# Performance work log

Measured on AMD Instinct MI355X. Metric: run time of the kernel, lower is better.

The kernel has to match this reference:

```python
import jax, jax.numpy as jnp
import numpy as np

M, B, S, D, H = 3, 32, 256, 768, 1024
LN_EPS = 1e-5


def _ln(x, g, b):
    m = jnp.mean(x, axis=-1, keepdims=True)
    v = jnp.mean((x - m) ** 2, axis=-1, keepdims=True)
    return (x - m) / jnp.sqrt(v + LN_EPS) * g + b


def setup_inputs() -> dict:
    key = jax.random.key(0)
    ks = jax.random.split(key, 16)
    sc = 0.02  # weight init scale
    return {
        "feats": jax.random.normal(ks[0], (M, B, S, D), jnp.float32),
        "Wq": jax.random.normal(ks[1], (M, D, D), jnp.float32) * sc,
        "bq": jnp.zeros((M, D), jnp.float32),
        "Wk": jax.random.normal(ks[2], (M, D, D), jnp.float32) * sc,
        "bk": jnp.zeros((M, D), jnp.float32),
        "Wv": jax.random.normal(ks[3], (M, D, D), jnp.float32) * sc,
        "bv": jnp.zeros((M, D), jnp.float32),
        "pgq_w": jax.random.normal(ks[4], (M, D), jnp.float32) * sc,
        "pgq_b": jnp.zeros((M,), jnp.float32),
        "pgk_w": jax.random.normal(ks[5], (M, D), jnp.float32) * sc,
        "pgk_b": jnp.zeros((M,), jnp.float32),
        "mu_w": jax.random.normal(ks[6], (M, D), jnp.float32) * sc,
        "mu_b": jnp.zeros((M,), jnp.float32),
        "lv_w": jax.random.normal(ks[7], (M, D), jnp.float32) * sc,
        "lv_b": jnp.zeros((M,), jnp.float32),
        "dyn": jnp.ones((1,), jnp.float32),
        "WE_w": jax.random.normal(ks[8], (M, D, D), jnp.float32) * sc,
        "WE_b": jnp.zeros((M, D), jnp.float32),
        "Wh_w": jax.random.normal(ks[9], (M, D, D), jnp.float32) * sc,
        "Wh_b": jnp.zeros((M, D), jnp.float32),
        "Wqc_w": jax.random.normal(ks[10], (M, D, D), jnp.float32) * sc,
        "Wqc_b": jnp.zeros((M, D), jnp.float32),
        "lnE_g": jnp.ones((M, D), jnp.float32),
        "lnE_b": jnp.zeros((M, D), jnp.float32),
        "lnG_g": jnp.ones((M, D), jnp.float32),
        "lnG_b": jnp.zeros((M, D), jnp.float32),
        "out_w": jax.random.normal(ks[11], (D * M, H), jnp.float32) * sc,
        "out_b": jnp.zeros((H,), jnp.float32),
        "eps": jax.random.normal(ks[12], (M, M - 1, B, S, 1), jnp.float32),
    }


def reference(feats, Wq, bq, Wk, bk, Wv, bv, pgq_w, pgq_b, pgk_w, pgk_b,
              mu_w, mu_b, lv_w, lv_b, dyn, WE_w, WE_b, Wh_w, Wh_b, Wqc_w, Wqc_b,
              lnE_g, lnE_b, lnG_g, lnG_b, out_w, out_b, eps):
    # batched per-modality projections: [M,B,S,D]
    Qs = jnp.einsum('mbsd,mde->mbse', feats, Wq) + bq[:, None, None, :]
    Ks = jnp.einsum('mbsd,mde->mbse', feats, Wk) + bk[:, None, None, :]
    Vs = jnp.einsum('mbsd,mde->mbse', feats, Wv) + bv[:, None, None, :]
    scale = 1.0 / jnp.sqrt(jnp.float32(D))

    kl = jnp.float32(0.0)
    outs = []
    for i in range(M):
        Qi = Qs[i]  # [B,S,D]
        mu = jnp.einsum('bsd,d->bs', Qi, mu_w[i])[..., None] + mu_b[i]      # [B,S,1]
        lv = jnp.einsum('bsd,d->bs', Qi, lv_w[i])[..., None] + lv_b[i]      # [B,S,1]
        std = jnp.exp(0.5 * lv)
        pq_base = jax.nn.sigmoid(
            jnp.einsum('bsd,d->bs', Qi, pgq_w[i])[..., None] + pgq_b[i])    # [B,S,1]
        kl_i = -0.5 * jnp.sum(1.0 + lv - mu ** 2 - jnp.exp(lv))
        agg = jnp.zeros_like(Qi)
        cnt = 0
        for j in range(M):
            if j == i:
                continue
            d_gate = mu + dyn * std * eps[i, cnt]  # reparameterization
            cnt += 1
            kl = kl + kl_i
            g = jax.nn.sigmoid(d_gate)             # [B,S,1]
            p_q = pq_base * g
            p_k = jax.nn.sigmoid(
                jnp.einsum('bsd,d->bs', Ks[j], pgk_w[i])[..., None] + pgk_b[i]) * g
            A = jnp.einsum('bqd,bkd->bqk', Qi, Ks[j]) * scale
            A = A * p_q * jnp.swapaxes(p_k, 1, 2)  # pregated scores
            W = jax.nn.softmax(A, axis=-1)
            agg = agg + jnp.einsum('bqk,bkd->bqd', W, Vs[j])
        # CAG
        E = jax.nn.relu(agg @ WE_w[i] + WE_b[i])
        G = jax.nn.relu(agg @ Wh_w[i] + Wh_b[i] + Qi @ Wqc_w[i] + Wqc_b[i])
        Ci = _ln(E, lnE_g[i], lnE_b[i]) * _ln(G, lnG_g[i], lnG_b[i])
        outs.append(Ci)
    fused = jnp.concatenate(outs, axis=-1)[:, 0, :]  # [B, M*D]
    out = fused @ out_w + out_b                       # [B, H]
    return out, kl
```

## Files before the change

### kernel.cpp

```cpp
#include <hip/hip_runtime.h>

#define M 3
#define B 32
#define S 256
#define D 768
#define H 1024
#define MD (M * D)
#define NP (M * (M - 1))
#define SCALE 0.03608439182435161f
#define LN_EPS 1e-5f

#define OFF_WMU   0
#define OFF_WLV   2304
#define OFF_WPGQ  4608
#define OFF_WPK   6912
#define OFF_CMU   11520
#define OFF_CLV   11523
#define OFF_CPGQ  11526
#define OFF_CPK   11529
#define OFF_MU    11552
#define OFF_LV    36128
#define OFF_PKPRE 60704
#define OFF_PQPRE 109856
#define OFF_Q     109952
#define OFF_QBK   183680
#define OFF_QK    183872
#define OFF_FSUM  331328
#define OFF_AGG   478784
#define OFF_E     552512
#define OFF_G     626240
#define OFF_FUSED 699968
#define OFF_KL    773696
#define OFF_WKT   773760
#define OFF_ARENA 2543232

__device__ __forceinline__ float wave_reduce(float v) {
    #pragma unroll
    for (int o = 32; o > 0; o >>= 1) v += __shfl_down(v, o, 64);
    return v;
}

__device__ __forceinline__ float sigmoidf(float x) {
    return 1.0f / (1.0f + __expf(-x));
}

__device__ __forceinline__ float dot4(float4 a, float4 b) {
    return a.x * b.x + a.y * b.y + a.z * b.z + a.w * b.w;
}

__device__ __forceinline__ void fma4(float4& a, float s, float4 w) {
    a.x += s * w.x; a.y += s * w.y; a.z += s * w.z; a.w += s * w.w;
}

__global__ __launch_bounds__(256) void k_prep(const float* Wq, const float* Wk,
        const float* bq, const float* bk,
        const float* mu_w, const float* mu_b, const float* lv_w, const float* lv_b,
        const float* pgq_w, const float* pgq_b, const float* pgk_w, const float* pgk_b,
        float* ws) {
    int blk = blockIdx.x;
    if (blk < 72) {
        int mat = blk / 12, rg = blk % 12;
        const float* Wm; const float *va, *vb, *vc;
        float *oa, *ob, *oc; int nv;
        if (mat < 3) {
            int i = mat;
            Wm = Wq + i * D * D;
            va = mu_w + i * D; vb = lv_w + i * D; vc = pgq_w + i * D;
            oa = ws + OFF_WMU + i * D; ob = ws + OFF_WLV + i * D; oc = ws + OFF_WPGQ + i * D;
            nv = 3;
        } else {
            int j = mat - 3;
            int i1 = (j == 0) ? 1 : 0, i2 = (j == 2) ? 1 : 2;
            int p1 = 2 * i1 + ((j < i1) ? j : j - 1);
            int p2 = 2 * i2 + ((j < i2) ? j : j - 1);
            Wm = Wk + j * D * D;
            va = pgk_w + i1 * D; vb = pgk_w + i2 * D; vc = va;
            oa = ws + OFF_WPK + p1 * D; ob = ws + OFF_WPK + p2 * D; oc = oa;
            nv = 2;
        }
        int wave = threadIdx.x >> 6, lane = threadIdx.x & 63;
        const float4* va4 = (const float4*)va;
        const float4* vb4 = (const float4*)vb;
        const float4* vc4 = (const float4*)vc;
        float4 A0 = va4[lane], A1 = va4[lane + 64], A2 = va4[lane + 128];
        float4 B0 = vb4[lane], B1 = vb4[lane + 64], B2 = vb4[lane + 128];
        float4 C0 = vc4[lane], C1 = vc4[lane + 64], C2 = vc4[lane + 128];
        int base = rg * 64 + wave * 16;
        for (int r = 0; r < 16; r += 2) {
            const float4* rowP = (const float4*)(Wm + (base + r) * D);
            const float4* rowQ = (const float4*)(Wm + (base + r + 1) * D);
            float4 x0 = rowP[lane], x1 = rowP[lane + 64], x2 = rowP[lane + 128];
            float4 y0 = rowQ[lane], y1 = rowQ[lane + 64], y2 = rowQ[lane + 128];
            float daP = dot4(x0, A0) + dot4(x1, A1) + dot4(x2, A2);
            float dbP = dot4(x0, B0) + dot4(x1, B1) + dot4(x2, B2);
            float dcP = dot4(x0, C0) + dot4(x1, C1) + dot4(x2, C2);
            float daQ = dot4(y0, A0) + dot4(y1, A1) + dot4(y2, A2);
            float dbQ = dot4(y0, B0) + dot4(y1, B1) + dot4(y2, B2);
            float dcQ = dot4(y0, C0) + dot4(y1, C1) + dot4(y2, C2);
            daP = wave_reduce(daP); dbP = wave_reduce(dbP);
            daQ = wave_reduce(daQ); dbQ = wave_reduce(dbQ);
            if (nv == 3) { dcP = wave_reduce(dcP); dcQ = wave_reduce(dcQ); }
            if (lane == 0) {
                oa[base + r] = daP; ob[base + r] = dbP;
                oa[base + r + 1] = daQ; ob[base + r + 1] = dbQ;
                if (nv == 3) { oc[base + r] = dcP; oc[base + r + 1] = dcQ; }
            }
        }
    } else if (blk < 87) {
        int job = blk - 72;
        const float *a, *bvec; float bias; float* out;
        if (job < 3)      { int i = job;     a = bq + i * D; bvec = mu_w + i * D;  bias = mu_b[i];  out = ws + OFF_CMU + i; }
        else if (job < 6) { int i = job - 3; a = bq + i * D; bvec = lv_w + i * D;  bias = lv_b[i];  out = ws + OFF_CLV + i; }
        else if (job < 9) { int i = job - 6; a = bq + i * D; bvec = pgq_w + i * D; bias = pgq_b[i]; out = ws + OFF_CPGQ + i; }
        else {
            int p = job - 9, i = p / 2, c = p % 2, j = c + (c >= i ? 1 : 0);
            a = bk + j * D; bvec = pgk_w + i * D; bias = pgk_b[i]; out = ws + OFF_CPK + p;
        }
        int t = threadIdx.x;
        float part = 0.f;
        if (t < 192) part = dot4(((const float4*)a)[t], ((const float4*)bvec)[t]);
        part = wave_reduce(part);
        __shared__ float r[4];
        if ((t & 63) == 0) r[t >> 6] = part;
        __syncthreads();
        if (t == 0) *out = r[0] + r[1] + r[2] + r[3] + bias;
    } else {
        int r = blk - 87;
        int j = r / 144; r = r % 144;
        int d0 = (r / 12) * 64, e0 = (r % 12) * 64;
        __shared__ float tile[64][65];
        const float* src = Wk + j * D * D;
        for (int idx = threadIdx.x; idx < 4096; idx += 256) {
            int rr = idx / 64, cc = idx % 64;
            tile[rr][cc] = src[(d0 + rr) * D + e0 + cc];
        }
        __syncthreads();
        float* dst = ws + OFF_WKT + j * D * D;
        for (int idx = threadIdx.x; idx < 4096; idx += 256) {
            int rr = idx / 64, cc = idx % 64;
            dst[(e0 + rr) * D + d0 + cc] = tile[cc][rr];
        }
    }
}

__global__ __launch_bounds__(256) void k_stats(const float* feats, float* ws) {
    __shared__ float klred[4];
    int wave = threadIdx.x >> 6, lane = threadIdx.x & 63;
    int m = blockIdx.x / 512;
    int row0 = blockIdx.x * 16 + wave * 4;
    int i1 = (m == 0) ? 1 : 0, i2 = (m == 2) ? 1 : 2;
    int p0 = 2 * i1 + ((m < i1) ? m : m - 1);
    int p1 = 2 * i2 + ((m < i2) ? m : m - 1);
    const float4* wmu  = (const float4*)(ws + OFF_WMU + m * D);
    const float4* wlv  = (const float4*)(ws + OFF_WLV + m * D);
    const float4* wpgq = (const float4*)(ws + OFF_WPGQ + m * D);
    const float4* wpk0 = (const float4*)(ws + OFF_WPK + p0 * D);
    const float4* wpk1 = (const float4*)(ws + OFF_WPK + p1 * D);
    float4 U0 = wmu[lane],  U1 = wmu[lane + 64],  U2 = wmu[lane + 128];
    float4 L0 = wlv[lane],  L1 = wlv[lane + 64],  L2 = wlv[lane + 128];
    float4 Q0 = wpgq[lane], Q1 = wpgq[lane + 64], Q2 = wpgq[lane + 128];
    float4 P0 = wpk0[lane], P1 = wpk0[lane + 64], P2 = wpk0[lane + 128];
    float4 R0 = wpk1[lane], R1 = wpk1[lane + 64], R2 = wpk1[lane + 128];
    float4 x[4][3];
    #pragma unroll
    for (int rr = 0; rr < 4; rr++) {
        const float4* f = (const float4*)(feats + (size_t)(row0 + rr) * D);
        x[rr][0] = f[lane]; x[rr][1] = f[lane + 64]; x[rr][2] = f[lane + 128];
    }
    float amu[4], alv[4], apgq[4], apk0[4], apk1[4];
    #pragma unroll
    for (int rr = 0; rr < 4; rr++) {
        amu[rr]  = dot4(x[rr][0], U0) + dot4(x[rr][1], U1) + dot4(x[rr][2], U2);
        alv[rr]  = dot4(x[rr][0], L0) + dot4(x[rr][1], L1) + dot4(x[rr][2], L2);
        apgq[rr] = dot4(x[rr][0], Q0) + dot4(x[rr][1], Q1) + dot4(x[rr][2], Q2);
        apk0[rr] = dot4(x[rr][0], P0) + dot4(x[rr][1], P1) + dot4(x[rr][2], P2);
        apk1[rr] = dot4(x[rr][0], R0) + dot4(x[rr][1], R1) + dot4(x[rr][2], R2);
    }
    #pragma unroll
    for (int rr = 0; rr < 4; rr++) {
        amu[rr] = wave_reduce(amu[rr]);  alv[rr] = wave_reduce(alv[rr]);
        apgq[rr] = wave_reduce(apgq[rr]);
        apk0[rr] = wave_reduce(apk0[rr]); apk1[rr] = wave_reduce(apk1[rr]);
    }
    if (lane == 0) {
        float cmu = ws[OFF_CMU + m], clv = ws[OFF_CLV + m];
        float cpgq = ws[OFF_CPGQ + m];
        float cpk0 = ws[OFF_CPK + p0], cpk1 = ws[OFF_CPK + p1];
        float klsum = 0.f;
        #pragma unroll
        for (int rr = 0; rr < 4; rr++) {
            int row = row0 + rr;
            int rem = row % (B * S);
            int b = rem / S, s = rem % S;
            float muv = amu[rr] + cmu;
            float lvv = alv[rr] + clv;
            ws[OFF_MU + row] = muv;
            ws[OFF_LV + row] = lvv;
            ws[OFF_PKPRE + (p0 * B + b) * S + s] = apk0[rr] + cpk0;
            ws[OFF_PKPRE + (p1 * B + b) * S + s] = apk1[rr] + cpk1;
            if (s == 0) ws[OFF_PQPRE + m * B + b] = apgq[rr] + cpgq;
            klsum += 1.0f + lvv - muv * muv - __expf(lvv);
        }
        klred[wave] = klsum;
    }
    __syncthreads();
    if (threadIdx.x == 0)
        atomicAdd(ws + OFF_KL, -(klred[0] + klred[1] + klred[2] + klred[3]));
}


__global__ __launch_bounds__(192) void k_qrow(const float* feats, const float* Wq, float* ws) {
    int blk = blockIdx.x;
    int i = blk / 96, r = blk % 96, bg = r / 24, kc = r % 24;
    int kbase = kc * 32;
    __shared__ __align__(16) float xs[32][8];
    for (int idx = threadIdx.x; idx < 256; idx += 192) {
        int d = idx / 8, bb = idx % 8;
        xs[d][bb] = feats[((size_t)(i * B + bg * 8 + bb) * S) * D + kbase + d];
    }
    __syncthreads();
    int e4 = threadIdx.x * 4;
    const float* Wm = Wq + i * D * D + kbase * D + e4;
    float4 acc[8];
    #pragma unroll
    for (int bb = 0; bb < 8; bb++) acc[bb] = make_float4(0.f, 0.f, 0.f, 0.f);
    for (int k = 0; k < 32; k++) {
        float4 w = *(const float4*)(Wm + k * D);
        float4 x0 = *(const float4*)&xs[k][0];
        float4 x1 = *(const float4*)&xs[k][4];
        fma4(acc[0], x0.x, w); fma4(acc[1], x0.y, w);
        fma4(acc[2], x0.z, w); fma4(acc[3], x0.w, w);
        fma4(acc[4], x1.x, w); fma4(acc[5], x1.y, w);
        fma4(acc[6], x1.z, w); fma4(acc[7], x1.w, w);
    }
    #pragma unroll
    for (int bb = 0; bb < 8; bb++)
        *(float4*)&ws[OFF_ARENA + kc * 73728 + (i * 32 + bg * 8 + bb) * 768 + e4] = acc[bb];
}

__global__ __launch_bounds__(256) void k_red_q(const float* bq, const float* bk, float* ws) {
    int blk = blockIdx.x;
    int i = blk / B, b = blk % B;
    int fbase = (i * B + b) * D;
    int t = threadIdx.x;
    __shared__ float4 qsh[192];
    __shared__ float redsh[8];
    if (t < 192) {
        float4 a = *(const float4*)&bq[i * D + t * 4];
        #pragma unroll
        for (int kc = 0; kc < 24; kc++) {
            float4 v = *(const float4*)&ws[OFF_ARENA + kc * 73728 + fbase + t * 4];
            a.x += v.x; a.y += v.y; a.z += v.z; a.w += v.w;
        }
        *(float4*)&ws[OFF_Q + fbase + t * 4] = a;
        qsh[t] = a;
    }
    __syncthreads();
    int jA = (i == 0) ? 1 : 0, jB = (i == 2) ? 1 : 2;
    float pA_ = 0.f, pB_ = 0.f;
    if (t < 192) {
        float4 q = qsh[t];
        pA_ = dot4(q, *(const float4*)&bk[jA * D + t * 4]);
        pB_ = dot4(q, *(const float4*)&bk[jB * D + t * 4]);
    }
    pA_ = wave_reduce(pA_); pB_ = wave_reduce(pB_);
    int wave = t >> 6, lane = t & 63;
    if (lane == 0) { redsh[wave] = pA_; redsh[4 + wave] = pB_; }
    __syncthreads();
    if (t == 0) {
        ws[OFF_QBK + (2 * i) * B + b]     = redsh[0] + redsh[1] + redsh[2] + redsh[3];
        ws[OFF_QBK + (2 * i + 1) * B + b] = redsh[4] + redsh[5] + redsh[6] + redsh[7];
    }
}

__global__ __launch_bounds__(192) void k_qk(float* ws) {
    int blk = blockIdx.x;
    int j = blk / 96, r = blk % 96, vg = r / 12, kc = r % 12;
    int kbase = kc * 64;
    int i1 = (j == 0) ? 1 : 0, i2 = (j == 2) ? 1 : 2;
    __shared__ __align__(16) float xs[64][8];
    for (int idx = threadIdx.x; idx < 512; idx += 192) {
        int d = idx / 8, v = idx % 8;
        int v64 = vg * 8 + v;
        int i_ = (v64 < 32) ? i1 : i2, b = v64 & 31;
        xs[d][v] = ws[OFF_Q + (i_ * 32 + b) * 768 + kbase + d];
    }
    __syncthreads();
    int e4 = threadIdx.x * 4;
    const float* Wm = ws + OFF_WKT + j * D * D + kbase * D + e4;
    float4 acc[8];
    #pragma unroll
    for (int bb = 0; bb < 8; bb++) acc[bb] = make_float4(0.f, 0.f, 0.f, 0.f);
// ... 299 lines not shown
    const float* gg = lnG_g + i * D; const float* gbv = lnG_b + i * D;
    o[t]       = ((e0 - mE) * sE * eg[t]       + ebv[t])       * ((g0 - mG) * sG * gg[t]       + gbv[t]);
    o[t + 256] = ((e1 - mE) * sE * eg[t + 256] + ebv[t + 256]) * ((g1 - mG) * sG * gg[t + 256] + gbv[t + 256]);
    o[t + 512] = ((e2 - mE) * sE * eg[t + 512] + ebv[t + 512]) * ((g2 - mG) * sG * gg[t + 512] + gbv[t + 512]);
}

__global__ __launch_bounds__(256) void k_out(const float* out_w, float* ws) {
    int blk = blockIdx.x;
    int bg = blk / 36, kc = blk % 36;
    int kbase = kc * 64;
    __shared__ __align__(16) float xs[64][8];
    for (int idx = threadIdx.x; idx < 512; idx += 256) {
        int d = idx / 8, bb = idx % 8;
        xs[d][bb] = ws[OFF_FUSED + (bg * 8 + bb) * MD + kbase + d];
    }
    __syncthreads();
    int e4 = threadIdx.x * 4;
    const float* Wm = out_w + kbase * H + e4;
    float4 acc[8];
    #pragma unroll
    for (int bb = 0; bb < 8; bb++) acc[bb] = make_float4(0.f, 0.f, 0.f, 0.f);
    for (int k = 0; k < 64; k++) {
        float4 w = *(const float4*)(Wm + k * H);
        float4 x0 = *(const float4*)&xs[k][0];
        float4 x1 = *(const float4*)&xs[k][4];
        fma4(acc[0], x0.x, w); fma4(acc[1], x0.y, w);
        fma4(acc[2], x0.z, w); fma4(acc[3], x0.w, w);
        fma4(acc[4], x1.x, w); fma4(acc[5], x1.y, w);
        fma4(acc[6], x1.z, w); fma4(acc[7], x1.w, w);
    }
    #pragma unroll
    for (int bb = 0; bb < 8; bb++)
        *(float4*)&ws[OFF_ARENA + kc * 32768 + (bg * 8 + bb) * 1024 + e4] = acc[bb];
}

__global__ __launch_bounds__(256) void k_fin(const float* out_b, float* ws, float* out) {
    int b = blockIdx.x;
    int h4 = threadIdx.x * 4;
    float4 a = *(const float4*)&out_b[h4];
    #pragma unroll
    for (int kc = 0; kc < 36; kc++) {
        float4 p = *(const float4*)&ws[OFF_ARENA + kc * 32768 + b * 1024 + h4];
        a.x += p.x; a.y += p.y; a.z += p.z; a.w += p.w;
    }
    *(float4*)&out[b * H + h4] = a;
    if (b == 0 && threadIdx.x == 0) out[B * H] = ws[OFF_KL];
}

extern "C" void kernel_launch(void* const* d_in, const int* in_sizes, int n_in,
                              void* d_out, int out_size, void* d_ws, size_t ws_size,
                              hipStream_t stream) {
    const float* feats = (const float*)d_in[0];
    const float* Wq    = (const float*)d_in[1];
    const float* bq    = (const float*)d_in[2];
    const float* Wk    = (const float*)d_in[3];
    const float* bk    = (const float*)d_in[4];
    const float* Wv    = (const float*)d_in[5];
    const float* bv    = (const float*)d_in[6];
    const float* pgq_w = (const float*)d_in[7];
    const float* pgq_b = (const float*)d_in[8];
    const float* pgk_w = (const float*)d_in[9];
    const float* pgk_b = (const float*)d_in[10];
    const float* mu_w  = (const float*)d_in[11];
    const float* mu_b  = (const float*)d_in[12];
    const float* lv_w  = (const float*)d_in[13];
    const float* lv_b  = (const float*)d_in[14];
    const float* dyn   = (const float*)d_in[15];
    const float* WE_w  = (const float*)d_in[16];
    const float* WE_b  = (const float*)d_in[17];
    const float* Wh_w  = (const float*)d_in[18];
    const float* Wh_b  = (const float*)d_in[19];
    const float* Wqc_w = (const float*)d_in[20];
    const float* Wqc_b = (const float*)d_in[21];
    const float* lnE_g = (const float*)d_in[22];
    const float* lnE_b = (const float*)d_in[23];
    const float* lnG_g = (const float*)d_in[24];
    const float* lnG_b = (const float*)d_in[25];
    const float* out_w = (const float*)d_in[26];
    const float* out_b = (const float*)d_in[27];
    const float* eps   = (const float*)d_in[28];
    float* ws  = (float*)d_ws;
    float* out = (float*)d_out;

    hipMemsetAsync((char*)d_ws + OFF_KL * sizeof(float), 0, sizeof(float), stream);

    k_prep<<<519, 256, 0, stream>>>(Wq, Wk, bq, bk, mu_w, mu_b, lv_w, lv_b,
                                    pgq_w, pgq_b, pgk_w, pgk_b, ws);
    k_stats<<<1536, 256, 0, stream>>>(feats, ws);
    k_qrow<<<288, 192, 0, stream>>>(feats, Wq, ws);
    k_red_q<<<96, 256, 0, stream>>>(bq, bk, ws);
    k_qk<<<288, 192, 0, stream>>>(ws);
    k_red_qk<<<144, 256, 0, stream>>>(ws);
    k_score<<<384, 256, 0, stream>>>(feats, ws);
    k_wsum<<<288, 256, 0, stream>>>(feats, eps, dyn, ws);
    k_agg<<<288, 192, 0, stream>>>(Wv, ws);
    k_red_agg<<<72, 256, 0, stream>>>(bv, ws);
    k_eg<<<288, 192, 0, stream>>>(WE_w, Wh_w, Wqc_w, ws);
    k_red_eg<<<144, 256, 0, stream>>>(WE_b, Wh_b, Wqc_b, ws);
    k_ln<<<M * B, 256, 0, stream>>>(lnE_g, lnE_b, lnG_g, lnG_b, ws);
    k_out<<<144, 256, 0, stream>>>(out_w, ws);
    k_fin<<<32, 256, 0, stream>>>(out_b, ws, out);
}
```

Baseline: 360.9 us.

## Fuse all stages into one cooperative persistent kernel with grid syncs

Replaces the chain of fifteen separate kernel launches with a single cooperative kernel that walks every former stage in grid-stride loops, separated by grid.sync barriers. It also folds the per-row statistics pass (mu, logvar, key-gate pre-activations, KL) into the score pass, so the large feats tensor is streamed once there instead of twice. The aim is to remove per-launch overhead and one full read of feats. The cost is fixed-size grid parallelism (512 blocks), grid-wide barrier latency between stages, and a fallback to the old launch chain if the cooperative launch fails.

```diff
diff --git a/kernel.cpp b/kernel.cpp
--- a/kernel.cpp
+++ b/kernel.cpp
@@ -1,4 +1,7 @@
 #include <hip/hip_runtime.h>
+#include <hip/hip_cooperative_groups.h>
+
+namespace cg = cooperative_groups;
 
 #define M 3
 #define B 32
@@ -51,6 +54,596 @@
 __device__ __forceinline__ void fma4(float4& a, float s, float4 w) {
     a.x += s * w.x; a.y += s * w.y; a.z += s * w.z; a.w += s * w.w;
 }
+
+struct MegaParams {
+    const float *feats, *Wq, *bq, *Wk, *bk, *Wv, *bv;
+    const float *pgq_w, *pgq_b, *pgk_w, *pgk_b;
+    const float *mu_w, *mu_b, *lv_w, *lv_b, *dyn;
+    const float *WE_w, *WE_b, *Wh_w, *Wh_b, *Wqc_w, *Wqc_b;
+    const float *lnE_g, *lnE_b, *lnG_g, *lnG_b, *out_w, *out_b, *eps;
+    float *ws, *out;
+};
+
+__global__ __launch_bounds__(256, 2) void k_mega(MegaParams p) {
+    cg::grid_group grid = cg::this_grid();
+    __shared__ __align__(16) char shraw[64 * 65 * 4];
+    float* ws = p.ws;
+    const int tid = threadIdx.x;
+    const int NB = gridDim.x;
+
+    if (blockIdx.x == 0 && tid == 0) ws[OFF_KL] = 0.f;
+
+    for (int vb = blockIdx.x; vb < 519; vb += NB) {
+        if (vb < 72) {
+            int mat = vb / 12, rg = vb % 12;
+            const float* Wm; const float *va, *vbv, *vc;
+            float *oa, *ob, *oc; int nv;
+            if (mat < 3) {
+                int i = mat;
+                Wm = p.Wq + i * D * D;
+                va = p.mu_w + i * D; vbv = p.lv_w + i * D; vc = p.pgq_w + i * D;
+                oa = ws + OFF_WMU + i * D; ob = ws + OFF_WLV + i * D; oc = ws + OFF_WPGQ + i * D;
+                nv = 3;
+            } else {
+                int j = mat - 3;
+                int i1 = (j == 0) ? 1 : 0, i2 = (j == 2) ? 1 : 2;
+                int p1 = 2 * i1 + ((j < i1) ? j : j - 1);
+                int p2 = 2 * i2 + ((j < i2) ? j : j - 1);
+                Wm = p.Wk + j * D * D;
+                va = p.pgk_w + i1 * D; vbv = p.pgk_w + i2 * D; vc = va;
+                oa = ws + OFF_WPK + p1 * D; ob = ws + OFF_WPK + p2 * D; oc = oa;
+                nv = 2;
+            }
+            int wave = tid >> 6, lane = tid & 63;
+            const float4* va4 = (const float4*)va;
+            const float4* vb4 = (const float4*)vbv;
+            const float4* vc4 = (const float4*)vc;
+            float4 A0 = va4[lane], A1 = va4[lane + 64], A2 = va4[lane + 128];
+            float4 B0 = vb4[lane], B1 = vb4[lane + 64], B2 = vb4[lane + 128];
+            float4 C0 = vc4[lane], C1 = vc4[lane + 64], C2 = vc4[lane + 128];
+            int base = rg * 64 + wave * 16;
+            for (int r = 0; r < 16; r += 2) {
+                const float4* rowP = (const float4*)(Wm + (base + r) * D);
+                const float4* rowQ = (const float4*)(Wm + (base + r + 1) * D);
+                float4 x0 = rowP[lane], x1 = rowP[lane + 64], x2 = rowP[lane + 128];
+                float4 y0 = rowQ[lane], y1 = rowQ[lane + 64], y2 = rowQ[lane + 128];
+                float daP = dot4(x0, A0) + dot4(x1, A1) + dot4(x2, A2);
+                float dbP = dot4(x0, B0) + dot4(x1, B1) + dot4(x2, B2);
+                float dcP = dot4(x0, C0) + dot4(x1, C1) + dot4(x2, C2);
+                float daQ = dot4(y0, A0) + dot4(y1, A1) + dot4(y2, A2);
+                float dbQ = dot4(y0, B0) + dot4(y1, B1) + dot4(y2, B2);
+                float dcQ = dot4(y0, C0) + dot4(y1, C1) + dot4(y2, C2);
+                daP = wave_reduce(daP); dbP = wave_reduce(dbP);
+                daQ = wave_reduce(daQ); dbQ = wave_reduce(dbQ);
+                if (nv == 3) { dcP = wave_reduce(dcP); dcQ = wave_reduce(dcQ); }
+                if (lane == 0) {
+                    oa[base + r] = daP; ob[base + r] = dbP;
+                    oa[base + r + 1] = daQ; ob[base + r + 1] = dbQ;
+                    if (nv == 3) { oc[base + r] = dcP; oc[base + r + 1] = dcQ; }
+                }
+            }
+        } else if (vb < 87) {
+            int job = vb - 72;
+            const float *a, *bvec; float bias; float* out;
+            if (job < 3)      { int i = job;     a = p.bq + i * D; bvec = p.mu_w + i * D;  bias = p.mu_b[i];  out = ws + OFF_CMU + i; }
+            else if (job < 6) { int i = job - 3; a = p.bq + i * D; bvec = p.lv_w + i * D;  bias = p.lv_b[i];  out = ws + OFF_CLV + i; }
+            else if (job < 9) { int i = job - 6; a = p.bq + i * D; bvec = p.pgq_w + i * D; bias = p.pgq_b[i]; out = ws + OFF_CPGQ + i; }
+            else {
+                int pp = job - 9, i = pp / 2, c = pp % 2, j = c + (c >= i ? 1 : 0);
+                a = p.bk + j * D; bvec = p.pgk_w + i * D; bias = p.pgk_b[i]; out = ws + OFF_CPK + pp;
+            }
+            float part = 0.f;
+            if (tid < 192) part = dot4(((const float4*)a)[tid], ((const float4*)bvec)[tid]);
+            part = wave_reduce(part);
+            float* rsh = (float*)shraw;
+            if ((tid & 63) == 0) rsh[tid >> 6] = part;
+            __syncthreads();
+            if (tid == 0) *out = rsh[0] + rsh[1] + rsh[2] + rsh[3] + bias;
+        } else {
+            int r = vb - 87;
+            int j = r / 144; r = r % 144;
+            int d0 = (r / 12) * 64, e0 = (r % 12) * 64;
+            float* tile = (float*)shraw;
+            const float* src = p.Wk + j * D * D;
+            for (int idx = tid; idx < 4096; idx += 256) {
+                int rr = idx / 64, cc = idx % 64;
+                tile[rr * 65 + cc] = src[(d0 + rr) * D + e0 + cc];
+            }
+            __syncthreads();
+            float* dst = ws + OFF_WKT + j * D * D;
+            for (int idx = tid; idx < 4096; idx += 256) {
+                int rr = idx / 64, cc = idx % 64;
+                dst[(e0 + rr) * D + d0 + cc] = tile[cc * 65 + rr];
+            }
+        }
+        __syncthreads();
+    }
+    grid.sync();
+
+    for (int vb = blockIdx.x; vb < 288; vb += NB) {
+        int i = vb / 96, r = vb % 96, bg = r / 24, kc = r % 24;
+        int kbase = kc * 32;
+        float* xs = (float*)shraw;
+        {
+            int d = tid / 8, bb = tid % 8;
+            xs[d * 8 + bb] = p.feats[((size_t)(i * B + bg * 8 + bb) * S) * D + kbase + d];
+        }
+        __syncthreads();
+        if (tid < 192) {
+            int e4 = tid * 4;
+            const float* Wm = p.Wq + i * D * D + kbase * D + e4;
+            float4 acc[8];
+            #pragma unroll
+            for (int bb = 0; bb < 8; bb++) acc[bb] = make_float4(0.f, 0.f, 0.f, 0.f);
+            for (int k = 0; k < 32; k++) {
+                float4 w = *(const float4*)(Wm + k * D);
+                float4 x0 = *(const float4*)&xs[k * 8];
+                float4 x1 = *(const float4*)&xs[k * 8 + 4];
+                fma4(acc[0], x0.x, w); fma4(acc[1], x0.y, w);
+                fma4(acc[2], x0.z, w); fma4(acc[3], x0.w, w);
+                fma4(acc[4], x1.x, w); fma4(acc[5], x1.y, w);
+                fma4(acc[6], x1.z, w); fma4(acc[7], x1.w, w);
+            }
+            #pragma unroll
+            for (int bb = 0; bb < 8; bb++)
+                *(float4*)&ws[OFF_ARENA + kc * 73728 + (i * 32 + bg * 8 + bb) * 768 + e4] = acc[bb];
+        }
+        __syncthreads();
+    }
+    grid.sync();
+
+    for (int vb = blockIdx.x; vb < 96; vb += NB) {
+        int i = vb / B, b = vb % B;
+        int fbase = (i * B + b) * D;
+        float4* qsh = (float4*)shraw;
+        float* redsh = (float*)(shraw + 192 * 16);
+        if (tid < 192) {
+            float4 a = *(const float4*)&p.bq[i * D + tid * 4];
+            #pragma unroll
+            for (int kc = 0; kc < 24; kc++) {
+                float4 v = *(const float4*)&ws[OFF_ARENA + kc * 73728 + fbase + tid * 4];
+                a.x += v.x; a.y += v.y; a.z += v.z; a.w += v.w;
+            }
+            *(float4*)&ws[OFF_Q + fbase + tid * 4] = a;
+            qsh[tid] = a;
+        }
+        __syncthreads();
+        int jA = (i == 0) ? 1 : 0, jB = (i == 2) ? 1 : 2;
+        float pA_ = 0.f, pB_ = 0.f;
+        if (tid < 192) {
+            float4 q = qsh[tid];
+            pA_ = dot4(q, *(const float4*)&p.bk[jA * D + tid * 4]);
+            pB_ = dot4(q, *(const float4*)&p.bk[jB * D + tid * 4]);
+        }
+        pA_ = wave_reduce(pA_); pB_ = wave_reduce(pB_);
+        int wave = tid >> 6, lane = tid & 63;
+        if (lane == 0) { redsh[wave] = pA_; redsh[4 + wave] = pB_; }
+        __syncthreads();
+        if (tid == 0) {
+            ws[OFF_QBK + (2 * i) * B + b]     = redsh[0] + redsh[1] + redsh[2] + redsh[3];
+            ws[OFF_QBK + (2 * i + 1) * B + b] = redsh[4] + redsh[5] + redsh[6] + redsh[7];
+        }
+        __syncthreads();
+    }
+    grid.sync();
+
+    for (int vb = blockIdx.x; vb < 288; vb += NB) {
+        int j = vb / 96, r = vb % 96, vg = r / 12, kc = r % 12;
+        int kbase = kc * 64;
+        int i1 = (j == 0) ? 1 : 0, i2 = (j == 2) ? 1 : 2;
+        float* xs = (float*)shraw;
+        for (int idx = tid; idx < 512; idx += 256) {
+            int d = idx / 8, v = idx % 8;
+            int v64 = vg * 8 + v;
+            int i_ = (v64 < 32) ? i1 : i2, b = v64 & 31;
+            xs[d * 8 + v] = ws[OFF_Q + (i_ * 32 + b) * 768 + kbase + d];
+        }
+        __syncthreads();
+        if (tid < 192) {
+            int e4 = tid * 4;
+            const float* Wm = ws + OFF_WKT + j * D * D + kbase * D + e4;
+            float4 acc[8];
+            #pragma unroll
+            for (int bb = 0; bb < 8; bb++) acc[bb] = make_float4(0.f, 0.f, 0.f, 0.f);
+            for (int k = 0; k < 64; k++) {
+                float4 w = *(const float4*)(Wm + k * D);
+                float4 x0 = *(const float4*)&xs[k * 8];
+                float4 x1 = *(const float4*)&xs[k * 8 + 4];
+                fma4(acc[0], x0.x, w); fma4(acc[1], x0.y, w);
+                fma4(acc[2], x0.z, w); fma4(acc[3], x0.w, w);
+                fma4(acc[4], x1.x, w); fma4(acc[5], x1.y, w);
+                fma4(acc[6], x1.z, w); fma4(acc[7], x1.w, w);
+            }
+            #pragma unroll
+            for (int v = 0; v < 8; v++)
+                *(float4*)&ws[OFF_ARENA + kc * 147456 + (j * 64 + vg * 8 + v) * 768 + e4] = acc[v];
+        }
+        __syncthreads();
+    }
+    grid.sync();
+
+    for (int vb = blockIdx.x; vb < 144; vb += NB) {
+        int idx = vb * 256 + tid;
+        int fidx = idx * 4;
+        int pp = fidx / 24576, rem = fidx % 24576;
+        int b = rem / 768, d = rem % 768;
+        int i = pp / 2, c = pp % 2, j = c + (c >= i ? 1 : 0);
+        int i1 = (j == 0) ? 1 : 0;
+        int iidx = (i == i1) ? 0 : 1;
+        int vg = iidx * 32 + b;
+        float4 a = make_float4(0.f, 0.f, 0.f, 0.f);
+        #pragma unroll
+        for (int kc = 0; kc < 12; kc++) {
+            float4 q = *(const float4*)&ws[OFF_ARENA + kc * 147456 + (j * 64 + vg) * 768 + d];
+            a.x += q.x; a.y += q.y; a.z += q.z; a.w += q.w;
+        }
+        *(float4*)&ws[OFF_QK + fidx] = a;
+    }
+    grid.sync();
+
+    for (int vb = blockIdx.x; vb < 384; vb += NB) {
+        int j = vb / 128, r = vb % 128, b = r / 4, kc = r % 4;
+        int i1 = (j == 0) ? 1 : 0, i2 = (j == 2) ? 1 : 2;
+        int pA = 2 * i1 + ((j < i1) ? j : j - 1);
+        int pB = 2 * i2 + ((j < i2) ? j : j - 1);
+        int wave = tid >> 6, lane = tid & 63;
+        const float4* qa4 = (const float4*)(ws + OFF_QK + (pA * B + b) * D);
+        const float4* qb4 = (const float4*)(ws + OFF_QK + (pB * B + b) * D);
+        float4 qA0 = qa4[lane], qA1 = qa4[lane + 64], qA2 = qa4[lane + 128];
+        float4 qB0 = qb4[lane], qB1 = qb4[lane + 64], qB2 = qb4[lane + 128];
+        const float4* wmu4 = (const float4*)(ws + OFF_WMU + j * D);
+        const float4* wlv4 = (const float4*)(ws + OFF_WLV + j * D);
+        const float4* wk04 = (const float4*)(ws + OFF_WPK + pA * D);
+        const float4* wk14 = (const float4*)(ws + OFF_WPK + pB * D);
+        float4 U0 = wmu4[lane], U1 = wmu4[lane + 64], U2 = wmu4[lane + 128];
+        float4 L0 = wlv4[lane], L1 = wlv4[lane + 64], L2 = wlv4[lane + 128];
+        float4 K00 = wk04[lane], K01 = wk04[lane + 64], K02 = wk04[lane + 128];
+        float4 K10 = wk14[lane], K11 = wk14[lane + 64], K12 = wk14[lane + 128];
+        const float* fb = p.feats + ((j * B + b) * S) * D;
+        float* scA = ws + OFF_ARENA + ((j * B + b) * 2) * S;
+        float* scB = scA + S;
+        float cmu = ws[OFF_CMU + j], clv = ws[OFF_CLV + j];
+        float cpk0 = ws[OFF_CPK + pA], cpk1 = ws[OFF_CPK + pB];
+        if (kc == 0 && wave == 0) {
+            const float4* wg4 = (const float4*)(ws + OFF_WPGQ + j * D);
+            const float4* f0 = (const float4*)fb;
+            float dd = dot4(f0[lane], wg4[lane]) + dot4(f0[lane + 64], wg4[lane + 64])
+                     + dot4(f0[lane + 128], wg4[lane + 128]);
+            dd = wave_reduce(dd);
+            if (lane == 0) ws[OFF_PQPRE + j * B + b] = dd + ws[OFF_CPGQ + j];
+        }
+        int k0 = kc * 64 + wave * 16;
+        float klsum = 0.f;
+        for (int k = k0; k < k0 + 16; k += 2) {
+            const float4* fA = (const float4*)(fb + k * D);
+            const float4* fB = (const float4*)(fb + (k + 1) * D);
+            float4 a0 = fA[lane], a1 = fA[lane + 64], a2 = fA[lane + 128];
+            float4 b0 = fB[lane], b1 = fB[lane + 64], b2 = fB[lane + 128];
+            float sa1 = dot4(a0, qA0) + dot4(a1, qA1) + dot4(a2, qA2);
+            float sb1 = dot4(a0, qB0) + dot4(a1, qB1) + dot4(a2, qB2);
+            float mu1 = dot4(a0, U0) + dot4(a1, U1) + dot4(a2, U2);
+            float lv1 = dot4(a0, L0) + dot4(a1, L1) + dot4(a2, L2);
+            float p01 = dot4(a0, K00) + dot4(a1, K01) + dot4(a2, K02);
+            float p11 = dot4(a0, K10) + dot4(a1, K11) + dot4(a2, K12);
+            float sa2 = dot4(b0, qA0) + dot4(b1, qA1) + dot4(b2, qA2);
+            float sb2 = dot4(b0, qB0) + dot4(b1, qB1) + dot4(b2, qB2);
+            float mu2 = dot4(b0, U0) + dot4(b1, U1) + dot4(b2, U2);
+            float lv2 = dot4(b0, L0) + dot4(b1, L1) + dot4(b2, L2);
+            float p02 = dot4(b0, K00) + dot4(b1, K01) + dot4(b2, K02);
+            float p12 = dot4(b0, K10) + dot4(b1, K11) + dot4(b2, K12);
+            sa1 = wave_reduce(sa1); sb1 = wave_reduce(sb1);
+            mu1 = wave_reduce(mu1); lv1 = wave_reduce(lv1);
+            p01 = wave_reduce(p01); p11 = wave_reduce(p11);
+            sa2 = wave_reduce(sa2); sb2 = wave_reduce(sb2);
+            mu2 = wave_reduce(mu2); lv2 = wave_reduce(lv2);
+            p02 = wave_reduce(p02); p12 = wave_reduce(p12);
+            if (lane == 0) {
+                scA[k] = sa1; scB[k] = sb1; scA[k + 1] = sa2; scB[k + 1] = sb2;
+                float m1 = mu1 + cmu, l1 = lv1 + clv;
+                float m2 = mu2 + cmu, l2 = lv2 + clv;
+                int row = (j * B + b) * S + k;
+                ws[OFF_MU + row] = m1;      ws[OFF_MU + row + 1] = m2;
+                ws[OFF_LV + row] = l1;      ws[OFF_LV + row + 1] = l2;
+                ws[OFF_PKPRE + (pA * B + b) * S + k]     = p01 + cpk0;
+                ws[OFF_PKPRE + (pA * B + b) * S + k + 1] = p02 + cpk0;
+                ws[OFF_PKPRE + (pB * B + b) * S + k]     = p11 + cpk1;
+                ws[OFF_PKPRE + (pB * B + b) * S + k + 1] = p12 + cpk1;
+                klsum += 2.0f + l1 + l2 - m1 * m1 - m2 * m2 - __expf(l1) - __expf(l2);
+            }
+        }
+        if (lane == 0) atomicAdd(ws + OFF_KL, -klsum);
+    }
+    grid.sync();
+
+    for (int vb = blockIdx.x; vb < 288; vb += NB) {
+        int j = vb / 96, r = vb % 96, b = r / 3, dc = r % 3;
+        int i1 = (j == 0) ? 1 : 0, i2 = (j == 2) ? 1 : 2;
+        int pA = 2 * i1 + ((j < i1) ? j : j - 1);
+        int pB = 2 * i2 + ((j < i2) ? j : j - 1);
+        float* sA = (float*)shraw;
+        float* sB = sA + 256;
+        float* redm = sB + 256;
+        int t = tid;
+        float dynv = p.dyn[0];
+        const float* rawA = ws + OFF_ARENA + ((j * B + b) * 2) * S;
+        const float* rawB = rawA + S;
+        {
+            float muk = ws[OFF_MU + (i1 * B + b) * S + t];
+            float lvk = ws[OFF_LV + (i1 * B + b) * S + t];
+            float ek  = p.eps[(pA * B + b) * S + t];
+            float g   = sigmoidf(muk + dynv * __expf(0.5f * lvk) * ek);
+            float pk  = sigmoidf(ws[OFF_PKPRE + (pA * B + b) * S + t]) * g;
+            float mu0 = ws[OFF_MU + (i1 * B + b) * S];
+            float lv0 = ws[OFF_LV + (i1 * B + b) * S];
+            float e0  = p.eps[(pA * B + b) * S];
+            float g0  = sigmoidf(mu0 + dynv * __expf(0.5f * lv0) * e0);
+            float pq  = sigmoidf(ws[OFF_PQPRE + i1 * B + b]) * g0;
+            float qbk = ws[OFF_QBK + pA * B + b];
+            sA[t] = (rawA[t] + qbk) * SCALE * pq * pk;
+            muk = ws[OFF_MU + (i2 * B + b) * S + t];
+            lvk = ws[OFF_LV + (i2 * B + b) * S + t];
+            ek  = p.eps[(pB * B + b) * S + t];
+            g   = sigmoidf(muk + dynv * __expf(0.5f * lvk) * ek);
+            pk  = sigmoidf(ws[OFF_PKPRE + (pB * B + b) * S + t]) * g;
+            mu0 = ws[OFF_MU + (i2 * B + b) * S];
+            lv0 = ws[OFF_LV + (i2 * B + b) * S];
+            e0  = p.eps[(pB * B + b) * S];
+            g0  = sigmoidf(mu0 + dynv * __expf(0.5f * lv0) * e0);
+            pq  = sigmoidf(ws[OFF_PQPRE + i2 * B + b]) * g0;
+            qbk = ws[OFF_QBK + pB * B + b];
+            sB[t] = (rawB[t] + qbk) * SCALE * pq * pk;
+        }
+        __syncthreads();
+        redm[t] = sA[t]; __syncthreads();
+        for (int st = 128; st > 0; st >>= 1) { if (t < st) redm[t] = fmaxf(redm[t], redm[t + st]); __syncthreads(); }
+        float mxA = redm[0]; __syncthreads();
+        float wA = __expf(sA[t] - mxA);
+        redm[t] = wA; __syncthreads();
+        for (int st = 128; st > 0; st >>= 1) { if (t < st) redm[t] += redm[t + st]; __syncthreads(); }
+        float sumA = redm[0]; __syncthreads();
+        sA[t] = wA / sumA;
+        __syncthreads();
+        redm[t] = sB[t]; __syncthreads();
+        for (int st = 128; st > 0; st >>= 1) { if (t < st) redm[t] = fmaxf(redm[t], redm[t + st]); __syncthreads(); }
+        float mxB = redm[0]; __syncthreads();
+        float wB = __expf(sB[t] - mxB);
+        redm[t] = wB; __syncthreads();
+        for (int st = 128; st > 0; st >>= 1) { if (t < st) redm[t] += redm[t + st]; __syncthreads(); }
+        float sumB = redm[0]; __syncthreads();
+        sB[t] = wB / sumB;
+        __syncthreads();
+        int dim = dc * 256 + t;
+        const float* fcol = p.feats + ((j * B + b) * S) * D + dim;
+        float accA = 0.f, accB = 0.f;
+        #pragma unroll 8
+        for (int k = 0; k < S; k++) {
+            float fv = fcol[k * D];
+            accA += sA[k] * fv;
+            accB += sB[k] * fv;
+        }
+        ws[OFF_FSUM + (pA * B + b) * D + dim] = accA;
+        ws[OFF_FSUM + (pB * B + b) * D + dim] = accB;
+        __syncthreads();
+    }
+    grid.sync();
+
+    for (int vb = blockIdx.x; vb < 288; vb += NB) {
+        int i = vb / 96, r = vb % 96, bg = r / 24, kc = r % 24;
+        int kbase = kc * 32;
+        int j0 = (i == 0) ? 1 : 0, j1 = (i == 2) ? 1 : 2;
+        int p0 = 2 * i, p1 = 2 * i + 1;
+        float* xs0 = (float*)shraw;
+        float* xs1 = xs0 + 256;
+        {
+            int d = tid / 8, bb = tid % 8;
+            xs0[d * 8 + bb] = ws[OFF_FSUM + (p0 * B + bg * 8 + bb) * D + kbase + d];
+            xs1[d * 8 + bb] = ws[OFF_FSUM + (p1 * B + bg * 8 + bb) * D + kbase + d];
+        }
+        __syncthreads();
+        if (tid < 192) {
+            int e4 = tid * 4;
+            const float* W0 = p.Wv + j0 * D * D + kbase * D + e4;
+            const float* W1 = p.Wv + j1 * D * D + kbase * D + e4;
+            float4 acc[8];
+            #pragma unroll
+            for (int bb = 0; bb < 8; bb++) acc[bb] = make_float4(0.f, 0.f, 0.f, 0.f);
+            for (int k = 0; k < 32; k++) {
+                float4 w0 = *(const float4*)(W0 + k * D);
+                float4 w1 = *(const float4*)(W1 + k * D);
+                float4 a0 = *(const float4*)&xs0[k * 8];
+                float4 a1 = *(const float4*)&xs0[k * 8 + 4];
+                float4 b0 = *(const float4*)&xs1[k * 8];
+                float4 b1 = *(const float4*)&xs1[k * 8 + 4];
+                fma4(acc[0], a0.x, w0); fma4(acc[1], a0.y, w0);
+                fma4(acc[2], a0.z, w0); fma4(acc[3], a0.w, w0);
+                fma4(acc[4], a1.x, w0); fma4(acc[5], a1.y, w0);
+                fma4(acc[6], a1.z, w0); fma4(acc[7], a1.w, w0);
+                fma4(acc[0], b0.x, w1); fma4(acc[1], b0.y, w1);
+                fma4(acc[2], b0.z, w1); fma4(acc[3], b0.w, w1);
+                fma4(acc[4], b1.x, w1); fma4(acc[5], b1.y, w1);
+                fma4(acc[6], b1.z, w1); fma4(acc[7], b1.w, w1);
+            }
+            #pragma unroll
+            for (int bb = 0; bb < 8; bb++)
+                *(float4*)&ws[OFF_ARENA + kc * 73728 + (i * 32 + bg * 8 + bb) * 768 + e4] = acc[bb];
+        }
+        __syncthreads();
+    }
+    grid.sync();
+
+    for (int vb = blockIdx.x; vb < 72; vb += NB) {
+        int idx = vb * 256 + tid;
+        int fidx = idx * 4;
+        int i = fidx / 24576, e = fidx % 768;
+        int j0 = (i == 0) ? 1 : 0, j1 = (i == 2) ? 1 : 2;
+        float4 b0 = *(const float4*)&p.bv[j0 * 768 + e];
+        float4 b1 = *(const float4*)&p.bv[j1 * 768 + e];
+        float4 a = make_float4(b0.x + b1.x, b0.y + b1.y, b0.z + b1.z, b0.w + b1.w);
+        #pragma unroll
+        for (int kc = 0; kc < 24; kc++) {
+            float4 q = *(const float4*)&ws[OFF_ARENA + kc * 73728 + fidx];
+            a.x += q.x; a.y += q.y; a.z += q.z; a.w += q.w;
+        }
+        *(float4*)&ws[OFF_AGG + fidx] = a;
+    }
+    grid.sync();
+
+    for (int vb = blockIdx.x; vb < 288; vb += NB) {
+        int kind = vb / 144, r = vb % 144;
+        int i = r / 48, r2 = r % 48, bg = r2 / 12, kc = r2 % 12;
+        int kbase = kc * 64;
+        float* xa = (float*)shraw;
+        float* xq = xa + 512;
+        for (int idx = tid; idx < 512; idx += 256) {
+            int d = idx / 8, bb = idx % 8;
+            xa[d * 8 + bb] = ws[OFF_AGG + (i * B + bg * 8 + bb) * D + kbase + d];
+            if (kind) xq[d * 8 + bb] = ws[OFF_Q + (i * B + bg * 8 + bb) * D + kbase + d];
+        }
+        __syncthreads();
+        if (tid < 192) {
+            int e4 = tid * 4;
+            float4 acc[8];
+            #pragma unroll
+            for (int bb = 0; bb < 8; bb++) acc[bb] = make_float4(0.f, 0.f, 0.f, 0.f);
+            if (kind == 0) {
+                const float* Wm = p.WE_w + i * D * D + kbase * D + e4;
+                for (int k = 0; k < 64; k++) {
+                    float4 w = *(const float4*)(Wm + k * D);
+                    float4 a0 = *(const float4*)&xa[k * 8];
+                    float4 a1 = *(const float4*)&xa[k * 8 + 4];
+                    fma4(acc[0], a0.x, w); fma4(acc[1], a0.y, w);
+                    fma4(acc[2], a0.z, w); fma4(acc[3], a0.w, w);
+                    fma4(acc[4], a1.x, w); fma4(acc[5], a1.y, w);
+                    fma4(acc[6], a1.z, w); fma4(acc[7], a1.w, w);
+                }
+            } else {
+                const float* Wh = p.Wh_w + i * D * D + kbase * D + e4;
+                const float* Wc = p.Wqc_w + i * D * D + kbase * D + e4;
+                for (int k = 0; k < 64; k++) {
+                    float4 wh = *(const float4*)(Wh + k * D);
+                    float4 wc = *(const float4*)(Wc + k * D);
+                    float4 a0 = *(const float4*)&xa[k * 8];
+                    float4 a1 = *(const float4*)&xa[k * 8 + 4];
+                    float4 q0 = *(const float4*)&xq[k * 8];
+                    float4 q1 = *(const float4*)&xq[k * 8 + 4];
+                    fma4(acc[0], a0.x, wh); fma4(acc[1], a0.y, wh);
+                    fma4(acc[2], a0.z, wh); fma4(acc[3], a0.w, wh);
+                    fma4(acc[4], a1.x, wh); fma4(acc[5], a1.y, wh);
+                    fma4(acc[6], a1.z, wh); fma4(acc[7], a1.w, wh);
+                    fma4(acc[0], q0.x, wc); fma4(acc[1], q0.y, wc);
+                    fma4(acc[2], q0.z, wc); fma4(acc[3], q0.w, wc);
+                    fma4(acc[4], q1.x, wc); fma4(acc[5], q1.y, wc);
+                    fma4(acc[6], q1.z, wc); fma4(acc[7], q1.w, wc);
+                }
+            }
+            int base = OFF_ARENA + (kind ? 884736 : 0) + kc * 73728;
+            #pragma unroll
+            for (int bb = 0; bb < 8; bb++)
+                *(float4*)&ws[base + (i * 32 + bg * 8 + bb) * 768 + e4] = acc[bb];
+        }
+        __syncthreads();
+    }
+    grid.sync();
+
+    for (int vb = blockIdx.x; vb < 144; vb += NB) {
+        bool isG = vb >= 72;
+        int idx = (isG ? vb - 72 : vb) * 256 + tid;
+        int fidx = idx * 4;
+        int i = fidx / 24576, e = fidx % 768;
+        float4 a;
+        const float* base = ws + OFF_ARENA + (isG ? 884736 : 0);
+        if (isG) {
+            float4 b0 = *(const float4*)&p.Wh_b[i * 768 + e];
+            float4 b1 = *(const float4*)&p.Wqc_b[i * 768 + e];
+            a = make_float4(b0.x + b1.x, b0.y + b1.y, b0.z + b1.z, b0.w + b1.w);
+        } else {
+            a = *(const float4*)&p.WE_b[i * 768 + e];
+        }
+        #pragma unroll
+        for (int kc = 0; kc < 12; kc++) {
+            float4 q = *(const float4*)&base[kc * 73728 + fidx];
+            a.x += q.x; a.y += q.y; a.z += q.z; a.w += q.w;
+        }
+        a.x = fmaxf(a.x, 0.f); a.y = fmaxf(a.y, 0.f); a.z = fmaxf(a.z, 0.f); a.w = fmaxf(a.w, 0.f);
+        *(float4*)&ws[(isG ? OFF_G : OFF_E) + fidx] = a;
+    }
+    grid.sync();
+
+    for (int vb = blockIdx.x; vb < 96; vb += NB) {
+        int i = vb / B, b = vb % B;
+        const float* E = ws + OFF_E + (i * B + b) * D;
+        const float* G = ws + OFF_G + (i * B + b) * D;
+        int t = tid;
+        float e0 = E[t], e1 = E[t + 256], e2 = E[t + 512];
+        float g0 = G[t], g1 = G[t + 256], g2 = G[t + 512];
+        float* r1 = (float*)shraw;
+        float* r2 = r1 + 256; float* r3 = r2 + 256; float* r4 = r3 + 256;
+        r1[t] = e0 + e1 + e2;
+        r2[t] = e0 * e0 + e1 * e1 + e2 * e2;
+        r3[t] = g0 + g1 + g2;
+        r4[t] = g0 * g0 + g1 * g1 + g2 * g2;
+        __syncthreads();
+        for (int st = 128; st > 0; st >>= 1) {
+            if (t < st) { r1[t] += r1[t + st]; r2[t] += r2[t + st]; r3[t] += r3[t + st]; r4[t] += r4[t + st]; }
+            __syncthreads();
+        }
+        float mE = r1[0] * (1.0f / D), vE = r2[0] * (1.0f / D) - mE * mE;
+        float mG = r3[0] * (1.0f / D), vG = r4[0] * (1.0f / D) - mG * mG;
+        float sE = rsqrtf(vE + LN_EPS), sG = rsqrtf(vG + LN_EPS);
+        float* o = ws + OFF_FUSED + b * MD + i * D;
+        const float* eg = p.lnE_g + i * D; const float* ebv = p.lnE_b + i * D;
+        const float* gg = p.lnG_g + i * D; const float* gbv = p.lnG_b + i * D;
+        o[t]       = ((e0 - mE) * sE * eg[t]       + ebv[t])       * ((g0 - mG) * sG * gg[t]       + gbv[t]);
+        o[t + 256] = ((e1 - mE) * sE * eg[t + 256] + ebv[t + 256]) * ((g1 - mG) * sG * gg[t + 256] + gbv[t + 256]);
+        o[t + 512] = ((e2 - mE) * sE * eg[t + 512] + ebv[t + 512]) * ((g2 - mG) * sG * gg[t + 512] + gbv[t + 512]);
+        __syncthreads();
+    }
+    grid.sync();
+
+    for (int vb = blockIdx.x; vb < 144; vb += NB) {
+        int bg = vb / 36, kc = vb % 36;
+        int kbase = kc * 64;
+        float* xs = (float*)shraw;
+        for (int idx = tid; idx < 512; idx += 256) {
+            int d = idx / 8, bb = idx % 8;
+            xs[d * 8 + bb] = ws[OFF_FUSED + (bg * 8 + bb) * MD + kbase + d];
+        }
+        __syncthreads();
+        int e4 = tid * 4;
+        const float* Wm = p.out_w + kbase * H + e4;
+        float4 acc[8];
+        #pragma unroll
+        for (int bb = 0; bb < 8; bb++) acc[bb] = make_float4(0.f, 0.f, 0.f, 0.f);
+        for (int k = 0; k < 64; k++) {
+            float4 w = *(const float4*)(Wm + k * H);
+            float4 x0 = *(const float4*)&xs[k * 8];
+            float4 x1 = *(const float4*)&xs[k * 8 + 4];
+            fma4(acc[0], x0.x, w); fma4(acc[1], x0.y, w);
+            fma4(acc[2], x0.z, w); fma4(acc[3], x0.w, w);
+            fma4(acc[4], x1.x, w); fma4(acc[5], x1.y, w);
+            fma4(acc[6], x1.z, w); fma4(acc[7], x1.w, w);
+        }
+        #pragma unroll
+        for (int bb = 0; bb < 8; bb++)
+            *(float4*)&ws[OFF_ARENA + kc * 32768 + (bg * 8 + bb) * 1024 + e4] = acc[bb];
+        __syncthreads();
+    }
+    grid.sync();
+
+    for (int vb = blockIdx.x; vb < 32; vb += NB) {
+        int b = vb;
+        int h4 = tid * 4;
+        float4 a = *(const float4*)&p.out_b[h4];
+        #pragma unroll
+        for (int kc = 0; kc < 36; kc++) {
+            float4 q = *(const float4*)&ws[OFF_ARENA + kc * 32768 + b * 1024 + h4];
+            a.x += q.x; a.y += q.y; a.z += q.z; a.w += q.w;
+        }
+        *(float4*)&p.out[b * H + h4] = a;
+        if (b == 0 && tid == 0) p.out[B * H] = ws[OFF_KL];
+    }
+}
+
 
 __global__ __launch_bounds__(256) void k_prep(const float* Wq, const float* Wk,
         const float* bq, const float* bk,
@@ -207,7 +800,6 @@
     if (threadIdx.x == 0)
         atomicAdd(ws + OFF_KL, -(klred[0] + klred[1] + klred[2] + klred[3]));
 }
-
 
 __global__ __launch_bounds__(192) void k_qrow(const float* feats, const float* Wq, float* ws) {
     int blk = blockIdx.x;
@@ -673,22 +1265,32 @@
     float* ws  = (float*)d_ws;
     float* out = (float*)d_out;
 
-    hipMemsetAsync((char*)d_ws + OFF_KL * sizeof(float), 0, sizeof(float), stream);
-
-    k_prep<<<519, 256, 0, stream>>>(Wq, Wk, bq, bk, mu_w, mu_b, lv_w, lv_b,
-                                    pgq_w, pgq_b, pgk_w, pgk_b, ws);
-    k_stats<<<1536, 256, 0, stream>>>(feats, ws);
-    k_qrow<<<288, 192, 0, stream>>>(feats, Wq, ws);
-    k_red_q<<<96, 256, 0, stream>>>(bq, bk, ws);
-    k_qk<<<288, 192, 0, stream>>>(ws);
-    k_red_qk<<<144, 256, 0, stream>>>(ws);
-    k_score<<<384, 256, 0, stream>>>(feats, ws);
-    k_wsum<<<288, 256, 0, stream>>>(feats, eps, dyn, ws);
-    k_agg<<<288, 192, 0, stream>>>(Wv, ws);
-    k_red_agg<<<72, 256, 0, stream>>>(bv, ws);
-    k_eg<<<288, 192, 0, stream>>>(WE_w, Wh_w, Wqc_w, ws);
-    k_red_eg<<<144, 256, 0, stream>>>(WE_b, Wh_b, Wqc_b, ws);
-    k_ln<<<M * B, 256, 0, stream>>>(lnE_g, lnE_b, lnG_g, lnG_b, ws);
-    k_out<<<144, 256, 0, stream>>>(out_w, ws);
-    k_fin<<<32, 256, 0, stream>>>(out_b, ws, out);
-}
+    MegaParams p = { feats, Wq, bq, Wk, bk, Wv, bv,
+                     pgq_w, pgq_b, pgk_w, pgk_b,
+                     mu_w, mu_b, lv_w, lv_b, dyn,
+                     WE_w, WE_b, Wh_w, Wh_b, Wqc_w, Wqc_b,
+                     lnE_g, lnE_b, lnG_g, lnG_b, out_w, out_b, eps,
+                     ws, out };
+    void* args[] = { &p };
+    hipError_t err = hipLaunchCooperativeKernel((const void*)k_mega, dim3(512), dim3(256),
+                                                args, 0, stream);
+    if (err != hipSuccess) {
+        hipMemsetAsync((char*)d_ws + OFF_KL * sizeof(float), 0, sizeof(float), stream);
+        k_prep<<<519, 256, 0, stream>>>(Wq, Wk, bq, bk, mu_w, mu_b, lv_w, lv_b,
+                                        pgq_w, pgq_b, pgk_w, pgk_b, ws);
+        k_stats<<<1536, 256, 0, stream>>>(feats, ws);
+        k_qrow<<<288, 192, 0, stream>>>(feats, Wq, ws);
+        k_red_q<<<96, 256, 0, stream>>>(bq, bk, ws);
+        k_qk<<<288, 192, 0, stream>>>(ws);
+        k_red_qk<<<144, 256, 0, stream>>>(ws);
+        k_score<<<384, 256, 0, stream>>>(feats, ws);
+        k_wsum<<<288, 256, 0, stream>>>(feats, eps, dyn, ws);
+        k_agg<<<288, 192, 0, stream>>>(Wv, ws);
+        k_red_agg<<<72, 256, 0, stream>>>(bv, ws);
+        k_eg<<<288, 192, 0, stream>>>(WE_w, Wh_w, Wqc_w, ws);
+        k_red_eg<<<144, 256, 0, stream>>>(WE_b, Wh_b, Wqc_b, ws);
+        k_ln<<<M * B, 256, 0, stream>>>(lnE_g, lnE_b, lnG_g, lnG_b, ws);
+        k_out<<<144, 256, 0, stream>>>(out_w, ws);
+        k_fin<<<32, 256, 0, stream>>>(out_b, ws, out);
+    }
+}
```

Measured after the change: 1.085 ms. 3.01x slower.
